# Optimization experiments

Measured on AMD Instinct MI355X. Metric: run time of the kernel, lower is better.

The kernel has to match this reference:

```python
import jax, jax.numpy as jnp
import numpy as np

B, N, D = 8, 1024, 768
H = 12
HD = D // H
LN_EPS = 1e-5
EPS = 1e-8


def setup_inputs() -> dict:
    key = jax.random.key(0)
    ks = jax.random.split(key, 16)
    s = 0.02
    return {
        "x": jax.random.normal(ks[0], (B, N, D), jnp.float32),
        "low_freq_feat": jax.random.normal(ks[1], (B, N, D), jnp.float32),
        "high_freq_feat": jax.random.normal(ks[2], (B, N, D), jnp.float32),
        "W_qkv_id": jax.random.normal(ks[3], (D, 3 * D), jnp.float32) * s,
        "W_qkv_attr": jax.random.normal(ks[4], (D, 3 * D), jnp.float32) * s,
        "W_fg_id": jax.random.normal(ks[5], (D, D), jnp.float32) * s,
        "b_fg_id": jnp.zeros((D,), jnp.float32),
        "W_fg_attr": jax.random.normal(ks[6], (D, D), jnp.float32) * s,
        "b_fg_attr": jnp.zeros((D,), jnp.float32),
        "W_proj_id": jax.random.normal(ks[7], (D, D), jnp.float32) * s,
        "b_proj_id": jnp.zeros((D,), jnp.float32),
        "W_proj_attr": jax.random.normal(ks[8], (D, D), jnp.float32) * s,
        "b_proj_attr": jnp.zeros((D,), jnp.float32),
        "ln_id_g": jnp.ones((D,), jnp.float32),
        "ln_id_b": jnp.zeros((D,), jnp.float32),
        "ln_attr_g": jnp.ones((D,), jnp.float32),
        "ln_attr_b": jnp.zeros((D,), jnp.float32),
        "ortho_temperature": jnp.float32(1.0),
        "freq_guide_strength": jnp.float32(0.3),
    }


def _layernorm(x, g, b):
    mu = x.mean(-1, keepdims=True)
    var = ((x - mu) ** 2).mean(-1, keepdims=True)
    return (x - mu) * jax.lax.rsqrt(var + LN_EPS) * g + b


def reference(x, low_freq_feat, high_freq_feat,
              W_qkv_id, W_qkv_attr,
              W_fg_id, b_fg_id, W_fg_attr, b_fg_attr,
              W_proj_id, b_proj_id, W_proj_attr, b_proj_attr,
              ln_id_g, ln_id_b, ln_attr_g, ln_attr_b,
              ortho_temperature, freq_guide_strength):
    b, n, d = x.shape
    scale = HD ** -0.5

    def split_qkv(t):
        t = t.reshape(b, n, 3, H, HD).transpose(2, 0, 3, 1, 4)
        return t[0], t[1], t[2]

    q_id, k_id, v_id = split_qkv(x @ W_qkv_id)
    q_at, k_at, v_at = split_qkv(x @ W_qkv_attr)

    fs = jax.nn.sigmoid(freq_guide_strength)
    low_g = (low_freq_feat @ W_fg_id + b_fg_id).reshape(b, n, H, HD).transpose(0, 2, 1, 3)
    high_g = (high_freq_feat @ W_fg_attr + b_fg_attr).reshape(b, n, H, HD).transpose(0, 2, 1, 3)
    v_id = v_id + fs * low_g
    v_at = v_at + fs * high_g

    def soft_attn(q, k):
        a = jnp.clip(jnp.einsum('bhnd,bhmd->bhnm', q, k) * scale, -20.0, 20.0)
        return jax.nn.softmax(a, axis=-1)

    attn_id = soft_attn(q_id, k_id)
    attn_at = soft_attn(q_at, k_at)

    # soft orthogonal mask (same mask for both branches)
    overlap = ((attn_id + EPS) * (attn_at + EPS)).sum(-1, keepdims=True)
    temp = jnp.clip(ortho_temperature, 0.1, 5.0)
    mask = jax.nn.sigmoid(-overlap * temp)

    def mask_renorm(a):
        m = a * mask
        m = m / (m.sum(-1, keepdims=True) + EPS)
        return jnp.where(jnp.isnan(m), jnp.zeros_like(m), m)

    attn_id = mask_renorm(attn_id)
    attn_at = mask_renorm(attn_at)

    def branch_out(a, v, W, bias, g, beta):
        o = jnp.einsum('bhnm,bhmd->bhnd', a, v).transpose(0, 2, 1, 3).reshape(b, n, d)
        return _layernorm(o @ W + bias, g, beta)

    id_features = branch_out(attn_id, v_id, W_proj_id, b_proj_id, ln_id_g, ln_id_b)
    attr_features = branch_out(attn_at, v_at, W_proj_attr, b_proj_attr, ln_attr_g, ln_attr_b)
    return (id_features, attr_features)
```

## Files before the change

### kernel.cpp

```cpp
#include <hip/hip_runtime.h>
#include <stdint.h>


typedef __attribute__((ext_vector_type(8))) _Float16 f16x8;
typedef __attribute__((ext_vector_type(4))) _Float16 f16x4;
typedef __attribute__((ext_vector_type(4))) float    f32x4;

__device__ __forceinline__ void g2l16(const void* g, void* l) {
  __builtin_amdgcn_global_load_lds(
      (const __attribute__((address_space(1))) void*)g,
      (__attribute__((address_space(3))) void*)l, 16, 0, 0);
}

#define BARX()   asm volatile("s_barrier" ::: "memory")
#define WAITV0() asm volatile("s_waitcnt vmcnt(0)" ::: "memory")

template <bool SWAP>
__device__ __forceinline__ void gemm192(const _Float16* __restrict__ A,
                                        const _Float16* __restrict__ Bt,
                                        int K, int m0, int n0,
                                        _Float16* As, _Float16* Bs,
                                        f32x4 (&acc)[4][6]) {
  const int tid = threadIdx.x;
  const int lane = tid & 63, w = tid >> 6;
  const int wm = (w >> 1) * 64, wn = (w & 1) * 96;
  const int l15 = lane & 15, quad = lane >> 4;
  const int srow = lane >> 2;
  const int scol = ((lane & 3) ^ ((lane >> 3) & 3)) * 8;
  const int rg = (quad ^ ((l15 >> 1) & 3)) * 8;
  const int KT = K >> 6;

  auto stage = [&](int t) {
    const int kc = t * 64;
    _Float16* Ab = As + (t & 1) * 16384;
    _Float16* Bb = Bs + (t & 1) * 12288;
#pragma unroll
    for (int h = 0; h < 2; h++)
#pragma unroll
      for (int i = 0; i < 2; i++) {
        int c = w * 2 + i;
        g2l16(A + (size_t)(m0 + c * 16 + srow) * K + kc + h * 32 + scol,
              Ab + h * 8192 + c * 512);
      }
#pragma unroll
    for (int i = 0; i < 3; i++) {
      int j = w * 3 + i;
      int hb = j / 12, cb = j % 12;
      g2l16(Bt + (size_t)(n0 + cb * 16 + srow) * K + kc + hb * 32 + scol,
            Bb + hb * 6144 + cb * 512);
    }
  };

#pragma unroll
  for (int mt = 0; mt < 4; mt++)
#pragma unroll
    for (int nt = 0; nt < 6; nt++) acc[mt][nt] = (f32x4){0.f, 0.f, 0.f, 0.f};

  stage(0);
  WAITV0();
  BARX();

  for (int t = 0; t < KT; t++) {
    const _Float16* as = As + (t & 1) * 16384;
    const _Float16* bs = Bs + (t & 1) * 12288;
    if (t + 1 < KT) stage(t + 1);
#pragma unroll
    for (int ks = 0; ks < 2; ks++) {
      f16x8 a[4], b[6];
#pragma unroll
      for (int mt = 0; mt < 4; mt++)
        a[mt] = *(const f16x8*)(as + ks * 8192 + (wm + mt * 16 + l15) * 32 + rg);
#pragma unroll
      for (int nt = 0; nt < 6; nt++)
        b[nt] = *(const f16x8*)(bs + ks * 6144 + (wn + nt * 16 + l15) * 32 + rg);
      __builtin_amdgcn_sched_barrier(0);
      __builtin_amdgcn_s_setprio(1);
#pragma unroll
      for (int mt = 0; mt < 4; mt++)
#pragma unroll
        for (int nt = 0; nt < 6; nt++)
          acc[mt][nt] = SWAP
              ? __builtin_amdgcn_mfma_f32_16x16x32_f16(b[nt], a[mt], acc[mt][nt], 0, 0, 0)
              : __builtin_amdgcn_mfma_f32_16x16x32_f16(a[mt], b[nt], acc[mt][nt], 0, 0, 0);
      __builtin_amdgcn_s_setprio(0);
      __builtin_amdgcn_sched_barrier(0);
    }
    WAITV0();
    BARX();
  }
}

__global__ __launch_bounds__(256) void k_cast3(const float* __restrict__ s0,
                                               const float* __restrict__ s1,
                                               const float* __restrict__ s2,
                                               _Float16* __restrict__ d0,
                                               _Float16* __restrict__ d1,
                                               _Float16* __restrict__ d2) {
  int blk = blockIdx.x;
  const float* s; _Float16* d;
  if (blk < 6144)       { s = s0; d = d0; }
  else if (blk < 12288) { s = s1; d = d1; blk -= 6144; }
  else                  { s = s2; d = d2; blk -= 12288; }
  int i = blk * 256 + threadIdx.x;
  float4 v = ((const float4*)s)[i];
  f16x4 o = {(_Float16)v.x, (_Float16)v.y, (_Float16)v.z, (_Float16)v.w};
  *(f16x4*)(d + (size_t)i * 4) = o;
}

__device__ __forceinline__ void tcast32(const float* __restrict__ src,
                                        _Float16* __restrict__ dst,
                                        int N, int n0, int k0) {
  __shared__ float t[32][33];
  int tr = threadIdx.x >> 5, tc = threadIdx.x & 31;
#pragma unroll
  for (int i = 0; i < 4; i++) {
    int r = tr + i * 8;
    t[r][tc] = src[(size_t)(k0 + r) * N + n0 + tc];
  }
  __syncthreads();
#pragma unroll
  for (int i = 0; i < 4; i++) {
    int r = tr + i * 8;
    dst[(size_t)(n0 + r) * 768 + k0 + tc] = (_Float16)t[tc][r];
  }
}

__global__ __launch_bounds__(256) void k_tcast_all(const float* __restrict__ Wq0,
                                                   const float* __restrict__ Wq1,
                                                   const float* __restrict__ W0,
                                                   const float* __restrict__ W1,
                                                   const float* __restrict__ W2,
                                                   const float* __restrict__ W3,
                                                   _Float16* __restrict__ Dq,
                                                   _Float16* __restrict__ D0,
                                                   _Float16* __restrict__ D1,
                                                   _Float16* __restrict__ D2,
                                                   _Float16* __restrict__ D3) {
  int blk = blockIdx.x;
  if (blk < 3456) {
    int half = blk / 1728, rem = blk % 1728;
    int xx = rem % 72, yy = rem / 72;
    tcast32(half ? Wq1 : Wq0, Dq + (size_t)half * 2304 * 768, 2304, xx * 32, yy * 32);
  } else {
    blk -= 3456;
    int q = blk / 576, rem = blk % 576;
    int xx = rem % 24, yy = rem / 24;
    const float* src; _Float16* d;
    if (q == 0)      { src = W0; d = D0; }
    else if (q == 1) { src = W1; d = D1; }
    else if (q == 2) { src = W2; d = D2; }
    else             { src = W3; d = D3; }
    tcast32(src, d, 768, xx * 32, yy * 32);
  }
}

__global__ __launch_bounds__(512, 2) void k_gemm_qkv(const _Float16* __restrict__ A,
                                                     const _Float16* __restrict__ Bt,
                                                     _Float16* __restrict__ Qb,
                                                     _Float16* __restrict__ Kb,
                                                     _Float16* __restrict__ Vtb) {
  __shared__ alignas(16) _Float16 As[32768], Bs[24576];
  f32x4 acc[4][6];
  int m0 = blockIdx.y * 256, n0 = blockIdx.x * 192;
  int br = n0 / 2304;
  int three = (n0 - br * 2304) / 768;
  int lane = threadIdx.x & 63, w = threadIdx.x >> 6;
  int wm = (w >> 1) * 64, wn = (w & 1) * 96, l15 = lane & 15, quad = lane >> 4;

  if (three == 2) {
    gemm192<false>(A, Bt, 768, m0, n0, As, Bs, acc);
#pragma unroll
    for (int mt = 0; mt < 4; mt++)
#pragma unroll
      for (int nt = 0; nt < 6; nt++) {
        int n = n0 + wn + nt * 16 + l15;
        int c = n - br * 2304 - 1536;
        int h = c >> 6, hd = c & 63;
        int m = m0 + wm + mt * 16 + quad * 4;
        int b = m >> 10, tok = m & 1023;
        size_t head = (size_t)(br * 96 + b * 12 + h);
        f32x4 v = acc[mt][nt];
        f16x4 o;
#pragma unroll
        for (int r = 0; r < 4; r++) o[r] = (_Float16)v[r];
        *(f16x4*)(Vtb + (head * 64 + hd) * 1024 + tok) = o;
      }
  } else {
    gemm192<true>(A, Bt, 768, m0, n0, As, Bs, acc);
    float qscl = (three == 0) ? 0.125f * 1.44269504f : 1.0f;
    _Float16* dst = (three == 0) ? Qb : Kb;
#pragma unroll
    for (int mt = 0; mt < 4; mt++)
#pragma unroll
      for (int nt = 0; nt < 6; nt++) {
        int m = m0 + wm + mt * 16 + l15;
        int n = n0 + wn + nt * 16 + quad * 4;
        int c = n - br * 2304 - three * 768;
        int h = c >> 6, hd = c & 63;
        int b = m >> 10, tok = m & 1023;
        size_t head = (size_t)(br * 96 + b * 12 + h);
        f32x4 v = acc[mt][nt];
        f16x4 o;
#pragma unroll
        for (int r = 0; r < 4; r++) o[r] = (_Float16)(v[r] * qscl);
        *(f16x4*)(dst + (head * 1024 + tok) * 64 + hd) = o;
      }
  }
}

__global__ __launch_bounds__(512, 2) void k_gemm_fgadd(const _Float16* __restrict__ Alo,
                                                       const _Float16* __restrict__ Ahi,
                                                       const _Float16* __restrict__ Bid,
                                                       const _Float16* __restrict__ Bat,
                                                       const float* __restrict__ bid,
                                                       const float* __restrict__ bat,
                                                       const float* __restrict__ fgs,
                                                       _Float16* __restrict__ Vtb) {
  __shared__ alignas(16) _Float16 As[32768], Bs[24576];
  f32x4 acc[4][6];
  int br = blockIdx.x >> 2;
  int n0 = (blockIdx.x & 3) * 192, m0 = blockIdx.y * 256;
  const _Float16* A = br ? Ahi : Alo;
  const _Float16* Bt = br ? Bat : Bid;
  const float* bias = br ? bat : bid;
  gemm192<false>(A, Bt, 768, m0, n0, As, Bs, acc);
  float fs = 1.f / (1.f + __expf(-fgs[0]));
  int lane = threadIdx.x & 63, w = threadIdx.x >> 6;
  int wm = (w >> 1) * 64, wn = (w & 1) * 96, l15 = lane & 15, quad = lane >> 4;
#pragma unroll
  for (int mt = 0; mt < 4; mt++)
#pragma unroll
    for (int nt = 0; nt < 6; nt++) {
      int c = n0 + wn + nt * 16 + l15;
      int h = c >> 6, hd = c & 63;
      int m = m0 + wm + mt * 16 + quad * 4;
      int b = m >> 10, tok = m & 1023;
      size_t head = (size_t)(br * 96 + b * 12 + h);
      float bv = bias[c];
      f32x4 v = acc[mt][nt];
      _Float16* p = Vtb + (head * 64 + hd) * 1024 + tok;
      f16x4 old = *(const f16x4*)p;
      f16x4 o;
#pragma unroll
      for (int r = 0; r < 4; r++)
        o[r] = (_Float16)((float)old[r] + fs * (v[r] + bv));
      *(f16x4*)p = o;
    }
}

__global__ __launch_bounds__(256, 3) void k_attn(const _Float16* __restrict__ Qb,
                                                 const _Float16* __restrict__ Kb,
                                                 const _Float16* __restrict__ Vtb,
                                                 _Float16* __restrict__ Ob) {
  __shared__ alignas(16) _Float16 Qs[128 * 64];
  __shared__ alignas(16) _Float16 Ks[128 * 64];
  __shared__ alignas(16) _Float16 Vts[64 * 128];
  int hl = blockIdx.x;
  int br = hl / 96, bh = hl % 96;
  int qbase = blockIdx.y * 128;
  const _Float16* Qh = Qb + (size_t)hl * 65536;
  const _Float16* Kh = Kb + (size_t)hl * 65536;
  const _Float16* Vth = Vtb + (size_t)hl * 65536;
  int lane = threadIdx.x & 63, w = threadIdx.x >> 6;
  int l15 = lane & 15, quad = lane >> 4;
  const int key7 = l15 & 7;

  {
    int rr = lane >> 3, sg = (lane & 7) ^ rr;
#pragma unroll
    for (int i = 0; i < 4; i++) {
      int c = w * 4 + i;
      g2l16(Qh + (size_t)(qbase + c * 8 + rr) * 64 + sg * 8, Qs + c * 512);
    }
  }
  auto stage_kv = [&](int n0) {
    int rr8 = lane >> 3, sg8 = ((lane & 7) ^ rr8) * 8;
    int rr16 = lane >> 4;
#pragma unroll
    for (int i = 0; i < 4; i++) {
      int c = w * 4 + i;
      g2l16(Kh + (size_t)(n0 + c * 8 + rr8) * 64 + sg8, Ks + c * 512);
      int vrow = c * 4 + rr16;
      int sg16 = ((lane & 15) ^ (vrow & 15)) * 8;
      g2l16(Vth + (size_t)vrow * 1024 + n0 + sg16, Vts + c * 512);
    }
  };
  stage_kv(0);

  f32x4 o[2][4];
#pragma unroll
  for (int qg = 0; qg < 2; qg++)
#pragma unroll
    for (int i = 0; i < 4; i++) o[qg][i] = (f32x4){0.f, 0.f, 0.f, 0.f};
  float rs0 = 0.f, rs1 = 0.f;
  f16x8 bq[2][2];
  const f32x4 zero = (f32x4){0.f, 0.f, 0.f, 0.f};
  const int g0 = (quad ^ key7) * 8, g1 = ((4 + quad) ^ key7) * 8;

  for (int kt = 0; kt < 8; kt++) {
    __syncthreads();
    if (kt == 0) {
#pragma unroll
      for (int qg = 0; qg < 2; qg++) {
        bq[qg][0] = *(const f16x8*)(Qs + (w * 32 + qg * 16 + l15) * 64 + g0);
        bq[qg][1] = *(const f16x8*)(Qs + (w * 32 + qg * 16 + l15) * 64 + g1);
      }
    }
    f32x4 c0, c1;
    {
      f16x8 a0 = *(const f16x8*)(Ks + l15 * 64 + g0);
      f16x8 a1 = *(const f16x8*)(Ks + l15 * 64 + g1);
      c0 = __builtin_amdgcn_mfma_f32_16x16x32_f16(a0, bq[0][0], zero, 0, 0, 0);
      c0 = __builtin_amdgcn_mfma_f32_16x16x32_f16(a1, bq[0][1], c0, 0, 0, 0);
      c1 = __builtin_amdgcn_mfma_f32_16x16x32_f16(a0, bq[1][0], zero, 0, 0, 0);
      c1 = __builtin_amdgcn_mfma_f32_16x16x32_f16(a1, bq[1][1], c1, 0, 0, 0);
    }
#pragma unroll
    for (int nt = 0; nt < 8; nt++) {
      f32x4 n0_, n1_;
      if (nt < 7) {
        f16x8 a0 = *(const f16x8*)(Ks + ((nt + 1) * 16 + l15) * 64 + g0);
        f16x8 a1 = *(const f16x8*)(Ks + ((nt + 1) * 16 + l15) * 64 + g1);
        n0_ = __builtin_amdgcn_mfma_f32_16x16x32_f16(a0, bq[0][0], zero, 0, 0, 0);
        n0_ = __builtin_amdgcn_mfma_f32_16x16x32_f16(a1, bq[0][1], n0_, 0, 0, 0);
        n1_ = __builtin_amdgcn_mfma_f32_16x16x32_f16(a0, bq[1][0], zero, 0, 0, 0);
        n1_ = __builtin_amdgcn_mfma_f32_16x16x32_f16(a1, bq[1][1], n1_, 0, 0, 0);
      }
      f16x4 pt0, pt1;
#pragma unroll
      for (int r = 0; r < 4; r++) {
        float p = __builtin_amdgcn_exp2f(c0[r]);
        rs0 += p; pt0[r] = (_Float16)p;
      }
#pragma unroll
      for (int r = 0; r < 4; r++) {
        float p = __builtin_amdgcn_exp2f(c1[r]);
        rs1 += p; pt1[r] = (_Float16)p;
      }
#pragma unroll
      for (int hdt = 0; hdt < 4; hdt++) {
        int g = ((2 * nt + (quad >> 1)) ^ l15) * 8 + (quad & 1) * 4;
        f16x4 av = *(const f16x4*)(Vts + (hdt * 16 + l15) * 128 + g);
        o[0][hdt] = __builtin_amdgcn_mfma_f32_16x16x16f16(av, pt0, o[0][hdt], 0, 0, 0);
        o[1][hdt] = __builtin_amdgcn_mfma_f32_16x16x16f16(av, pt1, o[1][hdt], 0, 0, 0);
      }
      if (nt < 7) { c0 = n0_; c1 = n1_; }
    }
    __syncthreads();
    if (kt < 7) stage_kv((kt + 1) * 128);
  }
  int b = bh / 12, h = bh % 12;
#pragma unroll
  for (int qg = 0; qg < 2; qg++) {
    float l = qg ? rs1 : rs0;
    l += __shfl_xor(l, 16);
    l += __shfl_xor(l, 32);
    float inv = 1.f / l;
    size_t rowb = ((size_t)br * 8192 + b * 1024 + qbase + w * 32 + qg * 16 + l15) * 768 +
                  h * 64;
#pragma unroll
    for (int hdt = 0; hdt < 4; hdt++) {
      f16x4 u;
#pragma unroll
      for (int r = 0; r < 4; r++) u[r] = (_Float16)(o[qg][hdt][r] * inv);
      *(f16x4*)(Ob + rowb + hdt * 16 + quad * 4) = u;
    }
  }
}

__global__ __launch_bounds__(512, 2) void k_gemm_proj2(const _Float16* __restrict__ Aid,
                                                       const _Float16* __restrict__ Aat,
                                                       const _Float16* __restrict__ Bid,
                                                       const _Float16* __restrict__ Bat,
                                                       _Float16* __restrict__ Yid,
                                                       _Float16* __restrict__ Yat) {
  __shared__ alignas(16) _Float16 As[32768], Bs[24576];
  f32x4 acc[4][6];
  int half = blockIdx.x >> 2;
  int n0 = (blockIdx.x & 3) * 192, m0 = blockIdx.y * 256;
  const _Float16* A = half ? Aat : Aid;
  const _Float16* Bt = half ? Bat : Bid;
  _Float16* Y = half ? Yat : Yid;
  gemm192<true>(A, Bt, 768, m0, n0, As, Bs, acc);
  int lane = threadIdx.x & 63, w = threadIdx.x >> 6;
  int wm = (w >> 1) * 64, wn = (w & 1) * 96, l15 = lane & 15, quad = lane >> 4;
#pragma unroll
  for (int mt = 0; mt < 4; mt++)
#pragma unroll
    for (int nt = 0; nt < 6; nt++) {
      int m = m0 + wm + mt * 16 + l15;
      int n = n0 + wn + nt * 16 + quad * 4;
      f32x4 v = acc[mt][nt];
      f16x4 o;
#pragma unroll
      for (int r = 0; r < 4; r++) o[r] = (_Float16)v[r];
      *(f16x4*)(Y + (size_t)m * 768 + n) = o;
    }
}

__global__ __launch_bounds__(256) void k_ln(const _Float16* __restrict__ Yid,
                                            const _Float16* __restrict__ Yat,
                                            const float* __restrict__ bp_id,
                                            const float* __restrict__ bp_at,
                                            const float* __restrict__ g_id,
                                            const float* __restrict__ be_id,
                                            const float* __restrict__ g_at,
                                            const float* __restrict__ be_at,
                                            float* __restrict__ out) {
  int w = threadIdx.x >> 6, lane = threadIdx.x & 63;
  int r = blockIdx.x * 4 + w;
  int br = r >> 13, m = r & 8191;
  const _Float16* Y = br ? Yat : Yid;
  const float* bp = br ? bp_at : bp_id;
  const float* g = br ? g_at : g_id;
  const float* be = br ? be_at : be_id;
  float v[12], sum = 0.f, sq = 0.f;
#pragma unroll
  for (int j = 0; j < 3; j++) {
    int c = j * 256 + lane * 4;
    f16x4 y = *(const f16x4*)(Y + (size_t)m * 768 + c);
    float4 bv = *(const float4*)(bp + c);
#pragma unroll
    for (int r2 = 0; r2 < 4; r2++) {
      float t = (float)y[r2] + ((const float*)&bv)[r2];
      v[j * 4 + r2] = t; sum += t; sq += t * t;
    }
  }
#pragma unroll
  for (int d = 1; d < 64; d <<= 1) { sum += __shfl_xor(sum, d); sq += __shfl_xor(sq, d); }
  float mu = sum * (1.f / 768.f);
  float var = sq * (1.f / 768.f) - mu * mu;
  float rstd = rsqrtf(var + 1e-5f);
  float* op = out + (size_t)br * 6291456 + (size_t)m * 768;
#pragma unroll
  for (int j = 0; j < 3; j++) {
    int c = j * 256 + lane * 4;
    float4 gv = *(const float4*)(g + c);
    float4 bev = *(const float4*)(be + c);
    float4 ov;
#pragma unroll
    for (int r2 = 0; r2 < 4; r2++)
      ((float*)&ov)[r2] = (v[j * 4 + r2] - mu) * rstd * ((const float*)&gv)[r2] +
                          ((const float*)&bev)[r2];
    *(float4*)(op + c) = ov;
  }
}

extern "C" void kernel_launch(void* const* d_in, const int* in_sizes, int n_in,
                              void* d_out, int out_size, void* d_ws, size_t ws_size,
                              hipStream_t stream) {
  const float* x       = (const float*)d_in[0];
  const float* lowf    = (const float*)d_in[1];
  const float* highf   = (const float*)d_in[2];
  const float* Wqkv_id = (const float*)d_in[3];
  const float* Wqkv_at = (const float*)d_in[4];
  const float* Wfg_id  = (const float*)d_in[5];
  const float* bfg_id  = (const float*)d_in[6];
  const float* Wfg_at  = (const float*)d_in[7];
  const float* bfg_at  = (const float*)d_in[8];
  const float* Wpr_id  = (const float*)d_in[9];
  const float* bpr_id  = (const float*)d_in[10];
  const float* Wpr_at  = (const float*)d_in[11];
  const float* bpr_at  = (const float*)d_in[12];
  const float* g_id    = (const float*)d_in[13];
  const float* be_id   = (const float*)d_in[14];
  const float* g_at    = (const float*)d_in[15];
  const float* be_at   = (const float*)d_in[16];
  const float* fgs     = (const float*)d_in[18];

  char* ws = (char*)d_ws;
  _Float16* x_f    = (_Float16*)(ws + 0);
  _Float16* low_f  = (_Float16*)(ws + 12582912);
  _Float16* high_f = (_Float16*)(ws + 25165824);
  _Float16* wqkvt  = (_Float16*)(ws + 37748736);
  _Float16* wfgidt = (_Float16*)(ws + 44826624);
  _Float16* wfgatt = (_Float16*)(ws + 46006272);
  _Float16* wpridt = (_Float16*)(ws + 47185920);
  _Float16* wpratt = (_Float16*)(ws + 48365568);
  _Float16* Qb     = (_Float16*)(ws + 74711040);
  _Float16* Kb     = (_Float16*)(ws + 99876864);
  _Float16* Vtb    = (_Float16*)(ws + 125042688);
  _Float16* Ob     = (_Float16*)(ws + 150208512);
  _Float16* Y_id   = (_Float16*)(ws + 0);
  _Float16* Y_at   = (_Float16*)(ws + 49545216);

  k_cast3<<<18432, 256, 0, stream>>>(x, lowf, highf, x_f, low_f, high_f);
  k_tcast_all<<<5760, 256, 0, stream>>>(Wqkv_id, Wqkv_at, Wfg_id, Wfg_at, Wpr_id, Wpr_at,
                                        wqkvt, wfgidt, wfgatt, wpridt, wpratt);
  k_gemm_qkv<<<dim3(24, 32), 512, 0, stream>>>(x_f, wqkvt, Qb, Kb, Vtb);
  k_gemm_fgadd<<<dim3(8, 32), 512, 0, stream>>>(low_f, high_f, wfgidt, wfgatt,
                                                bfg_id, bfg_at, fgs, Vtb);
  k_attn<<<dim3(192, 8), 256, 0, stream>>>(Qb, Kb, Vtb, Ob);
  k_gemm_proj2<<<dim3(8, 32), 512, 0, stream>>>(Ob, Ob + 6291456, wpridt, wpratt,
                                                Y_id, Y_at);
  k_ln<<<4096, 256, 0, stream>>>(Y_id, Y_at, bpr_id, bpr_at, g_id, be_id, g_at, be_at,
                                 (float*)d_out);
}
```

Measured before the change: 434.3 us.

## Interleave LDS reads, global prefetch and MFMA in four barrier-synced GEMM phases

Restructures the 192-wide GEMM inner loop into four phases, each loading a subset of A/B fragments from LDS and then issuing 12 MFMAs. The global-to-LDS prefetch for the next tile is split into separate A and B parts placed between phases, and global addresses are precomputed outside the loop. The goal is to interleave memory traffic with matrix math and cut register pressure by holding only three B fragments at once. The cost is many extra block-wide barriers per K step, which can stall warps.

```diff
diff --git a/kernel.cpp b/kernel.cpp
--- a/kernel.cpp
+++ b/kernel.cpp
@@ -14,6 +14,21 @@
 
 #define BARX()   asm volatile("s_barrier" ::: "memory")
 #define WAITV0() asm volatile("s_waitcnt vmcnt(0)" ::: "memory")
+#define LGKM0()  asm volatile("s_waitcnt lgkmcnt(0)" ::: "memory")
+#define SB0()    __builtin_amdgcn_sched_barrier(0)
+
+#define MFMA12(NB)                                                            \
+  __builtin_amdgcn_s_setprio(1);                                              \
+  _Pragma("unroll")                                                           \
+  for (int mt = 0; mt < 4; mt++)                                              \
+    _Pragma("unroll")                                                         \
+    for (int i = 0; i < 3; i++)                                               \
+      acc[mt][(NB) + i] = SWAP                                                \
+          ? __builtin_amdgcn_mfma_f32_16x16x32_f16(b[i], a[mt],               \
+                                                   acc[mt][(NB) + i], 0, 0, 0)\
+          : __builtin_amdgcn_mfma_f32_16x16x32_f16(a[mt], b[i],               \
+                                                   acc[mt][(NB) + i], 0, 0, 0);\
+  __builtin_amdgcn_s_setprio(0);
 
 template <bool SWAP>
 __device__ __forceinline__ void gemm192(const _Float16* __restrict__ A,
@@ -28,27 +43,33 @@
   const int srow = lane >> 2;
   const int scol = ((lane & 3) ^ ((lane >> 3) & 3)) * 8;
   const int rg = (quad ^ ((l15 >> 1) & 3)) * 8;
+  const int rdA = (wm + l15) * 32 + rg;
+  const int rdB = (wn + l15) * 32 + rg;
   const int KT = K >> 6;
 
-  auto stage = [&](int t) {
+  const _Float16* gA0 = A + (size_t)(m0 + (w * 2) * 16 + srow) * K + scol;
+  const _Float16* gA1 = gA0 + (size_t)16 * K;
+  const _Float16* gB[3]; int lB[3];
+#pragma unroll
+  for (int i = 0; i < 3; i++) {
+    int j = w * 3 + i, hb = j / 12, cb = j % 12;
+    gB[i] = Bt + (size_t)(n0 + cb * 16 + srow) * K + hb * 32 + scol;
+    lB[i] = hb * 6144 + cb * 512;
+  }
+
+  auto stageA = [&](int t) {
     const int kc = t * 64;
-    _Float16* Ab = As + (t & 1) * 16384;
+    _Float16* Ab = As + (t & 1) * 16384 + w * 1024;
+    g2l16(gA0 + kc,      Ab);
+    g2l16(gA0 + kc + 32, Ab + 8192);
+    g2l16(gA1 + kc,      Ab + 512);
+    g2l16(gA1 + kc + 32, Ab + 8704);
+  };
+  auto stageB = [&](int t) {
+    const int kc = t * 64;
     _Float16* Bb = Bs + (t & 1) * 12288;
 #pragma unroll
-    for (int h = 0; h < 2; h++)
-#pragma unroll
-      for (int i = 0; i < 2; i++) {
-        int c = w * 2 + i;
-        g2l16(A + (size_t)(m0 + c * 16 + srow) * K + kc + h * 32 + scol,
-              Ab + h * 8192 + c * 512);
-      }
-#pragma unroll
-    for (int i = 0; i < 3; i++) {
-      int j = w * 3 + i;
-      int hb = j / 12, cb = j % 12;
-      g2l16(Bt + (size_t)(n0 + cb * 16 + srow) * K + kc + hb * 32 + scol,
-            Bb + hb * 6144 + cb * 512);
-    }
+    for (int i = 0; i < 3; i++) g2l16(gB[i] + kc, Bb + lB[i]);
   };
 
 #pragma unroll
@@ -56,35 +77,51 @@
 #pragma unroll
     for (int nt = 0; nt < 6; nt++) acc[mt][nt] = (f32x4){0.f, 0.f, 0.f, 0.f};
 
-  stage(0);
+  stageA(0); stageB(0);
   WAITV0();
   BARX();
 
   for (int t = 0; t < KT; t++) {
     const _Float16* as = As + (t & 1) * 16384;
     const _Float16* bs = Bs + (t & 1) * 12288;
-    if (t + 1 < KT) stage(t + 1);
-#pragma unroll
-    for (int ks = 0; ks < 2; ks++) {
-      f16x8 a[4], b[6];
-#pragma unroll
-      for (int mt = 0; mt < 4; mt++)
-        a[mt] = *(const f16x8*)(as + ks * 8192 + (wm + mt * 16 + l15) * 32 + rg);
-#pragma unroll
-      for (int nt = 0; nt < 6; nt++)
-        b[nt] = *(const f16x8*)(bs + ks * 6144 + (wn + nt * 16 + l15) * 32 + rg);
-      __builtin_amdgcn_sched_barrier(0);
-      __builtin_amdgcn_s_setprio(1);
-#pragma unroll
-      for (int mt = 0; mt < 4; mt++)
-#pragma unroll
-        for (int nt = 0; nt < 6; nt++)
-          acc[mt][nt] = SWAP
-              ? __builtin_amdgcn_mfma_f32_16x16x32_f16(b[nt], a[mt], acc[mt][nt], 0, 0, 0)
-              : __builtin_amdgcn_mfma_f32_16x16x32_f16(a[mt], b[nt], acc[mt][nt], 0, 0, 0);
-      __builtin_amdgcn_s_setprio(0);
-      __builtin_amdgcn_sched_barrier(0);
-    }
+    const bool st = (t + 1 < KT);
+    f16x8 a[4], b[3];
+
+#pragma unroll
+    for (int mt = 0; mt < 4; mt++) a[mt] = *(const f16x8*)(as + rdA + mt * 512);
+#pragma unroll
+    for (int i = 0; i < 3; i++) b[i] = *(const f16x8*)(bs + rdB + i * 512);
+    if (st) stageA(t + 1);
+    BARX(); LGKM0(); SB0();
+    MFMA12(0);
+    SB0();
+    BARX();
+
+#pragma unroll
+    for (int i = 0; i < 3; i++) b[i] = *(const f16x8*)(bs + rdB + (3 + i) * 512);
+    if (st) stageB(t + 1);
+    BARX(); LGKM0(); SB0();
+    MFMA12(3);
+    SB0();
+    BARX();
+
+#pragma unroll
+    for (int mt = 0; mt < 4; mt++)
+      a[mt] = *(const f16x8*)(as + 8192 + rdA + mt * 512);
+#pragma unroll
+    for (int i = 0; i < 3; i++)
+      b[i] = *(const f16x8*)(bs + 6144 + rdB + i * 512);
+    BARX(); LGKM0(); SB0();
+    MFMA12(0);
+    SB0();
+    BARX();
+
+#pragma unroll
+    for (int i = 0; i < 3; i++)
+      b[i] = *(const f16x8*)(bs + 6144 + rdB + (3 + i) * 512);
+    BARX(); LGKM0(); SB0();
+    MFMA12(3);
+    SB0();
     WAITV0();
     BARX();
   }
```

Measured after the change: 395.7 us. 1.1x faster.
